# Optimization experiments

Measured on AMD Instinct MI355X. Metric: run time of the kernel, lower is better.

Reference implementation:

```python
import jax, jax.numpy as jnp
import numpy as np

N_NODES = 100000
N_EDGES = 600000
DIM = 128

def setup_inputs() -> dict:
    key = jax.random.key(0)
    k1, k2, k3, k4 = jax.random.split(key, 4)
    node_emb = jax.random.normal(k1, (N_NODES, DIM), dtype=jnp.float32)
    rel_emb = jax.random.normal(k2, (N_EDGES, DIM), dtype=jnp.float32)
    src = jax.random.randint(k3, (N_EDGES,), 0, N_NODES, dtype=jnp.int64)
    dst = jax.random.randint(k4, (N_EDGES,), 0, N_NODES, dtype=jnp.int64)
    return {"node_emb": node_emb, "rel_emb": rel_emb, "src": src, "dst": dst}

def reference(node_emb, rel_emb, src, dst):
    # DistMult edge score: sum_d head[d] * rel[d] * tail[d]
    head = node_emb[src]            # [E, D] gather
    tail = node_emb[dst]            # [E, D] gather
    score = jnp.sum(head * rel_emb * tail, axis=-1)  # [E]
    return score
```

## Files before the change

### kernel.cpp

```cpp
#include <hip/hip_runtime.h>


#define DIM 128
#define EDGES_PER_BLOCK 8

__global__ __launch_bounds__(256) void distmult_score_kernel(
    const float* __restrict__ node_emb,
    const float* __restrict__ rel_emb,
    const int*   __restrict__ src,
    const int*   __restrict__ dst,
    float*       __restrict__ out,
    int E)
{
    const int tid    = threadIdx.x;
    const int half   = tid >> 5;
    const int lane32 = tid & 31;

    const int e = blockIdx.x * EDGES_PER_BLOCK + half;
    if (e >= E) return;

    const int s = src[e];
    const int d = dst[e];

    const float4* __restrict__ hp = (const float4*)(node_emb + (long long)s * DIM);
    const float4* __restrict__ tp = (const float4*)(node_emb + (long long)d * DIM);
    const float4* __restrict__ rp = (const float4*)(rel_emb  + (long long)e * DIM);

    const float4 h = hp[lane32];
    const float4 r = rp[lane32];
    const float4 t = tp[lane32];

    float v = h.x * r.x * t.x
            + h.y * r.y * t.y
            + h.z * r.z * t.z
            + h.w * r.w * t.w;

    #pragma unroll
    for (int off = 16; off > 0; off >>= 1)
        v += __shfl_xor(v, off, 32);

    if (lane32 == 0) out[e] = v;
}

extern "C" void kernel_launch(void* const* d_in, const int* in_sizes, int n_in,
                              void* d_out, int out_size, void* d_ws, size_t ws_size,
                              hipStream_t stream) {
    const float* node_emb = (const float*)d_in[0];
    const float* rel_emb  = (const float*)d_in[1];
    const int*   src      = (const int*)d_in[2];
    const int*   dst      = (const int*)d_in[3];
    float*       out      = (float*)d_out;

    const int E = in_sizes[2];

    const int grid = (E + EDGES_PER_BLOCK - 1) / EDGES_PER_BLOCK;
    distmult_score_kernel<<<grid, 256, 0, stream>>>(node_emb, rel_emb, src, dst, out, E);
}
```

Measured before the change: 458.4 us.

## Process four edges per 32-lane group with batched loads and merged reduction

Each 32-lane group now handles four consecutive edges, issuing all index, relation and node-row loads up front to raise memory-level parallelism. Relation rows are read and scores written with nontemporal hints so the streamed data does not pollute cache. The four per-edge reductions are merged into a transpose-style shuffle tree to cut shuffle count. This costs more registers per thread and a quarter as many blocks, plus a scalar tail path.

```diff
diff --git a/kernel.cpp b/kernel.cpp
--- a/kernel.cpp
+++ b/kernel.cpp
@@ -2,7 +2,11 @@
 
 
 #define DIM 128
-#define EDGES_PER_BLOCK 8
+#define U 4
+#define GROUPS 8
+#define EDGES_PER_BLOCK (U * GROUPS)
+
+typedef float f4 __attribute__((ext_vector_type(4)));
 
 __global__ __launch_bounds__(256) void distmult_score_kernel(
     const float* __restrict__ node_emb,
@@ -12,34 +16,85 @@
     float*       __restrict__ out,
     int E)
 {
-    const int tid    = threadIdx.x;
-    const int half   = tid >> 5;
-    const int lane32 = tid & 31;
+    const int tid  = threadIdx.x;
+    const int grp  = tid >> 5;
+    const int lane = tid & 31;
 
-    const int e = blockIdx.x * EDGES_PER_BLOCK + half;
-    if (e >= E) return;
+    const int e0 = (blockIdx.x * GROUPS + grp) * U;
+    if (e0 >= E) return;
 
-    const int s = src[e];
-    const int d = dst[e];
+    if (e0 + U <= E) {
+        int s[U], d[U];
+        #pragma unroll
+        for (int u = 0; u < U; ++u) {
+            s[u] = src[e0 + u];
+            d[u] = dst[e0 + u];
+        }
 
-    const float4* __restrict__ hp = (const float4*)(node_emb + (long long)s * DIM);
-    const float4* __restrict__ tp = (const float4*)(node_emb + (long long)d * DIM);
-    const float4* __restrict__ rp = (const float4*)(rel_emb  + (long long)e * DIM);
+        f4 r[U];
+        #pragma unroll
+        for (int u = 0; u < U; ++u) {
+            const f4* rp = (const f4*)(rel_emb + (size_t)(e0 + u) * DIM);
+            r[u] = __builtin_nontemporal_load(rp + lane);
+        }
 
-    const float4 h = hp[lane32];
-    const float4 r = rp[lane32];
-    const float4 t = tp[lane32];
+        f4 h[U], t[U];
+        #pragma unroll
+        for (int u = 0; u < U; ++u) {
+            const f4* hp = (const f4*)(node_emb + (size_t)s[u] * DIM);
+            const f4* tp = (const f4*)(node_emb + (size_t)d[u] * DIM);
+            h[u] = hp[lane];
+            t[u] = tp[lane];
+        }
 
-    float v = h.x * r.x * t.x
-            + h.y * r.y * t.y
-            + h.z * r.z * t.z
-            + h.w * r.w * t.w;
+        float v[U];
+        #pragma unroll
+        for (int u = 0; u < U; ++u) {
+            v[u] = h[u].x * r[u].x * t[u].x
+                 + h[u].y * r[u].y * t[u].y
+                 + h[u].z * r[u].z * t[u].z
+                 + h[u].w * r[u].w * t[u].w;
+        }
 
-    #pragma unroll
-    for (int off = 16; off > 0; off >>= 1)
-        v += __shfl_xor(v, off, 32);
-
-    if (lane32 == 0) out[e] = v;
+        #pragma unroll
+        for (int u = 0; u < U; ++u)
+            v[u] += __shfl_xor(v[u], 16, 32);
+        float a = (lane & 16) ? v[1] : v[0];
+        float b = (lane & 16) ? v[3] : v[2];
+        a += __shfl_xor(a, 8, 32);
+        b += __shfl_xor(b, 8, 32);
+        float c = (lane & 8) ? b : a;
+        c += __shfl_xor(c, 4, 32);
+        c += __shfl_xor(c, 2, 32);
+        c += __shfl_xor(c, 1, 32);
+        if ((lane & 7) == 0) {
+            int u;
+            if      (lane == 0)  u = 0;
+            else if (lane == 8)  u = 2;
+            else if (lane == 16) u = 1;
+            else                 u = 3;
+            __builtin_nontemporal_store(c, out + e0 + u);
+        }
+    } else {
+        for (int u = 0; u < U; ++u) {
+            const int e = e0 + u;
+            if (e >= E) break;
+            const int s = src[e];
+            const int d = dst[e];
+            const f4* hp = (const f4*)(node_emb + (size_t)s * DIM);
+            const f4* tp = (const f4*)(node_emb + (size_t)d * DIM);
+            const f4* rp = (const f4*)(rel_emb  + (size_t)e * DIM);
+            const f4 h = hp[lane];
+            const f4 r = rp[lane];
+            const f4 t = tp[lane];
+            float v = h.x * r.x * t.x + h.y * r.y * t.y
+                    + h.z * r.z * t.z + h.w * r.w * t.w;
+            #pragma unroll
+            for (int off = 16; off > 0; off >>= 1)
+                v += __shfl_xor(v, off, 32);
+            if (lane == 0) out[e] = v;
+        }
+    }
 }
 
 extern "C" void kernel_launch(void* const* d_in, const int* in_sizes, int n_in,
```

Result: slower. 472.2 us (+3.0%).

## Use persistent grid-stride blocks with software-pipelined prefetch of edge rows

Applied to the files above, without the earlier changes.

Replaces the one-edge-per-group launch with a fixed grid of 2048 blocks in which each 32-lane group walks edges with a grid stride. The loop fetches the next edge's rel/head/tail rows, and the indices two edges ahead, while it reduces the current edge, so gather latency overlaps with compute. This gives up the latency hiding that came from many short-lived waves and adds register pressure. Fewer resident groups could limit memory-level parallelism on this bandwidth-bound gather.

```diff
diff --git a/kernel.cpp b/kernel.cpp
--- a/kernel.cpp
+++ b/kernel.cpp
@@ -2,7 +2,10 @@
 
 
 #define DIM 128
-#define EDGES_PER_BLOCK 8
+#define GROUPS 8
+#define NBLOCKS 2048
+
+typedef float f4 __attribute__((ext_vector_type(4)));
 
 __global__ __launch_bounds__(256) void distmult_score_kernel(
     const float* __restrict__ node_emb,
@@ -12,34 +15,50 @@
     float*       __restrict__ out,
     int E)
 {
-    const int tid    = threadIdx.x;
-    const int half   = tid >> 5;
-    const int lane32 = tid & 31;
+    const int tid  = threadIdx.x;
+    const int grp  = tid >> 5;
+    const int lane = tid & 31;
 
-    const int e = blockIdx.x * EDGES_PER_BLOCK + half;
-    if (e >= E) return;
+    const int NG = gridDim.x * GROUPS;
+    int e0 = blockIdx.x * GROUPS + grp;
+    if (e0 >= E) return;
 
-    const int s = src[e];
-    const int d = dst[e];
+    int s0 = src[e0];
+    int d0 = dst[e0];
+    f4 r0 = ((const f4*)(rel_emb + (size_t)e0 * DIM))[lane];
+    f4 h0 = ((const f4*)(node_emb + (size_t)s0 * DIM))[lane];
+    f4 t0 = ((const f4*)(node_emb + (size_t)d0 * DIM))[lane];
 
-    const float4* __restrict__ hp = (const float4*)(node_emb + (long long)s * DIM);
-    const float4* __restrict__ tp = (const float4*)(node_emb + (long long)d * DIM);
-    const float4* __restrict__ rp = (const float4*)(rel_emb  + (long long)e * DIM);
+    int e1 = e0 + NG;
+    bool m1 = (e1 < E);
+    int s1 = 0, d1 = 0;
+    if (m1) { s1 = src[e1]; d1 = dst[e1]; }
 
-    const float4 h = hp[lane32];
-    const float4 r = rp[lane32];
-    const float4 t = tp[lane32];
+    while (true) {
+        f4 r1, h1, t1;
+        if (m1) {
+            r1 = ((const f4*)(rel_emb + (size_t)e1 * DIM))[lane];
+            h1 = ((const f4*)(node_emb + (size_t)s1 * DIM))[lane];
+            t1 = ((const f4*)(node_emb + (size_t)d1 * DIM))[lane];
+        }
+        const int e2 = e1 + NG;
+        const bool m2 = m1 && (e2 < E);
+        int s2 = 0, d2 = 0;
+        if (m2) { s2 = src[e2]; d2 = dst[e2]; }
 
-    float v = h.x * r.x * t.x
-            + h.y * r.y * t.y
-            + h.z * r.z * t.z
-            + h.w * r.w * t.w;
+        float v = h0.x * r0.x * t0.x
+                + h0.y * r0.y * t0.y
+                + h0.z * r0.z * t0.z
+                + h0.w * r0.w * t0.w;
+        #pragma unroll
+        for (int off = 16; off > 0; off >>= 1)
+            v += __shfl_xor(v, off, 32);
+        if (lane == 0) out[e0] = v;
 
-    #pragma unroll
-    for (int off = 16; off > 0; off >>= 1)
-        v += __shfl_xor(v, off, 32);
-
-    if (lane32 == 0) out[e] = v;
+        if (!m1) break;
+        e0 = e1; r0 = r1; h0 = h1; t0 = t1;
+        e1 = e2; s1 = s2; d1 = d2; m1 = m2;
+    }
 }
 
 extern "C" void kernel_launch(void* const* d_in, const int* in_sizes, int n_in,
@@ -53,6 +72,5 @@
 
     const int E = in_sizes[2];
 
-    const int grid = (E + EDGES_PER_BLOCK - 1) / EDGES_PER_BLOCK;
-    distmult_score_kernel<<<grid, 256, 0, stream>>>(node_emb, rel_emb, src, dst, out, E);
+    distmult_score_kernel<<<NBLOCKS, 256, 0, stream>>>(node_emb, rel_emb, src, dst, out, E);
 }
```

Measured after the change: 464.4 us. Within noise of the previous version (+1.3%).
